# Optimization experiments

Measured on AMD Instinct MI355X. Metric: run time of the kernel, lower is better.

Reference implementation:

```python
import jax, jax.numpy as jnp
import numpy as np

B, S, D, E = 4, 2048, 512, 32

def setup_inputs() -> dict:
    key = jax.random.key(0)
    k1, k2, k3 = jax.random.split(key, 3)
    x = jax.random.normal(k1, (B, S, D), dtype=jnp.float32)
    # glorot-ish scaling for weights
    gate_w = jax.random.normal(k2, (D, E), dtype=jnp.float32) * (1.0 / np.sqrt(D))
    gate_b = jnp.zeros((E,), dtype=jnp.float32)
    expert_w = jax.random.normal(k3, (E, D, D), dtype=jnp.float32) * (1.0 / np.sqrt(D))
    return {"x": x, "gate_w": gate_w, "gate_b": gate_b, "expert_w": expert_w}

def reference(x, gate_w, gate_b, expert_w):
    # gate_scores: [B,S,E] (context=None -> route on x itself)
    gate = jax.nn.softmax(jnp.einsum('bsd,de->bse', x, gate_w) + gate_b, axis=-1)
    # Dense soft-MoE: sum_e gate[b,s,e] * (x[b,s,:] @ expert_w[e])
    # Single einsum avoids materializing the [B,S,E,D] intermediate.
    out = jnp.einsum('bse,bsd,edf->bsf', gate, x, expert_w)
    return out
```

## Files before the change

### kernel.cpp

```cpp
#include <hip/hip_runtime.h>

#define TOK 8192
#define DIM 512
#define NE  32
#define KTOT (NE * DIM)

#define BM 128
#define BN 64
#define BK 64

typedef float f32x4 __attribute__((ext_vector_type(4)));
typedef short s16x8 __attribute__((ext_vector_type(8)));

typedef const void __attribute__((address_space(1)))* gp1_t;
typedef void __attribute__((address_space(3)))* lp3_t;

__device__ __forceinline__ void gl_lds16(const void* g, void* l) {
    __builtin_amdgcn_global_load_lds((gp1_t)g, (lp3_t)l, 16, 0, 0);
}

__device__ __forceinline__ ushort f2bf(float f) {
    unsigned u = __builtin_bit_cast(unsigned, f);
    unsigned r = (u + 0x7fffu + ((u >> 16) & 1u)) >> 16;
    return (ushort)r;
}

__global__ __launch_bounds__(256) void k_prep(const float* __restrict__ w,
                                              ushort* __restrict__ wt,
                                              const float* __restrict__ x,
                                              const float* __restrict__ gw,
                                              const float* __restrict__ gb,
                                              float* __restrict__ G2,
                                              ushort* __restrict__ xb) {
    __shared__ __align__(16) char smem[64 * 65 * 4];
    const int bx = blockIdx.x;
    const int tid = threadIdx.x;
    if (bx < 2048) {
        float (*tile)[65] = (float(*)[65])smem;
        const int e = bx >> 6;
        const int f0 = ((bx >> 3) & 7) * 64;
        const int d0 = (bx & 7) * 64;
        const int tx = tid & 63, ty = tid >> 6;
        const float* we = w + (size_t)e * DIM * DIM;
#pragma unroll
        for (int i = ty; i < 64; i += 4)
            tile[i][tx] = we[(size_t)(d0 + i) * DIM + f0 + tx];
        __syncthreads();
#pragma unroll
        for (int i = ty; i < 64; i += 4)
            wt[(size_t)(f0 + i) * KTOT + e * DIM + d0 + tx] = f2bf(tile[tx][i]);
    } else {
        float* xs = (float*)smem;
        const int t0 = (bx - 2048) * 8;
        const float* xBase = x + (size_t)t0 * DIM;
#pragma unroll
        for (int k = 0; k < 4; ++k) {
            int i4 = (k * 256 + tid) * 4;
            float4 v = *(const float4*)(xBase + i4);
            xs[i4 + 0] = v.x; xs[i4 + 1] = v.y; xs[i4 + 2] = v.z; xs[i4 + 3] = v.w;
            ushort4 o;
            o.x = f2bf(v.x); o.y = f2bf(v.y); o.z = f2bf(v.z); o.w = f2bf(v.w);
            *(ushort4*)(xb + (size_t)t0 * DIM + i4) = o;
        }
        __syncthreads();
        const int tok = tid >> 5;
        const int e = tid & 31;
        float l = gb[e];
        const float* xr = xs + tok * DIM;
#pragma unroll 8
        for (int d = 0; d < DIM; ++d)
            l += xr[d] * gw[d * NE + e];
        float mx = l;
#pragma unroll
        for (int m = 16; m >= 1; m >>= 1) mx = fmaxf(mx, __shfl_xor(mx, m));
        float ex = expf(l - mx);
        float s = ex;
#pragma unroll
        for (int m = 16; m >= 1; m >>= 1) s += __shfl_xor(s, m);
        G2[(size_t)e * TOK + t0 + tok] = ex / s;
    }
}

__global__ __launch_bounds__(256, 4) void k_moe_gemm(const ushort* __restrict__ xb,
                                                     const ushort* __restrict__ wt,
                                                     const float* __restrict__ G2,
                                                     float* __restrict__ out0,
                                                     float* __restrict__ out1) {
    __shared__ __align__(16) ushort Bs[2][BN * BK];
    __shared__ float Gs[16][BM];

    const int tid = threadIdx.x;
    const int m0 = blockIdx.y * BM;
    const int n0 = blockIdx.x * BN;
    const int e0 = blockIdx.z * 16;
    float* __restrict__ dst = blockIdx.z ? out1 : out0;

    for (int i = tid; i < 16 * BM; i += 256) {
        int e = i >> 7, r = i & 127;
        Gs[e][r] = G2[(size_t)(e0 + e) * TOK + m0 + r];
    }

    const int lane = tid & 63;
    const int wave = tid >> 6;
    const int wm = (wave & 1) * 64;
    const int wn = (wave >> 1) * 32;
    const int l15 = lane & 15;
    const int q = lane >> 4;
    const int keyR = l15 & 7;

    int rb[2][2];
#pragma unroll
    for (int j = 0; j < 2; ++j)
#pragma unroll
        for (int ks = 0; ks < 2; ++ks)
            rb[j][ks] = (wn + j * 16 + l15) * 128 + (((ks * 4 + q) ^ keyR) << 4);

    const int srow = tid >> 3;
    const int c8 = tid & 7;
    const int scol = ((c8 ^ (srow & 7)) * 8);
    const ushort* bBase = wt + (size_t)(n0 + srow) * KTOT + (size_t)e0 * DIM + scol;
    const ushort* bBase2 = bBase + (size_t)32 * KTOT;
    const int ldsOff = tid * 16;

    const ushort* aP[4];
#pragma unroll
    for (int i = 0; i < 4; ++i)
        aP[i] = xb + (size_t)(m0 + wm + i * 16 + l15) * DIM + q * 8;

    const f32x4 zv = {0.f, 0.f, 0.f, 0.f};
    f32x4 acc[4][2];
#pragma unroll
    for (int i = 0; i < 4; ++i)
#pragma unroll
        for (int j = 0; j < 2; ++j) acc[i][j] = zv;

    gl_lds16(bBase, (char*)Bs[0] + ldsOff);
    gl_lds16(bBase2, (char*)Bs[0] + 4096 + ldsOff);
    __syncthreads();

#pragma unroll 1
    for (int kt = 0; kt < 8; ++kt) {
        s16x8 a[4][2];
#pragma unroll
        for (int i = 0; i < 4; ++i) {
            a[i][0] = *(const s16x8*)(aP[i] + kt * 64);
            a[i][1] = *(const s16x8*)(aP[i] + kt * 64 + 32);
        }

#pragma unroll 1
        for (int ee = 0; ee < 16; ++ee) {
            const int g = kt * 16 + ee;
            if (g + 1 < 128) {
                const int gn = g + 1;
                const ushort* bN = bBase + (size_t)(gn & 15) * DIM + (gn >> 4) * BK;
                char* bL = (char*)Bs[gn & 1] + ldsOff;
                gl_lds16(bN, bL);
                gl_lds16(bN + (size_t)32 * KTOT, bL + 4096);
            }

            const char* Bb = (const char*)Bs[g & 1];
            s16x8 b[2][2];
#pragma unroll
            for (int j = 0; j < 2; ++j) {
                b[j][0] = *(const s16x8*)(Bb + rb[j][0]);
                b[j][1] = *(const s16x8*)(Bb + rb[j][1]);
            }

#pragma unroll
            for (int i = 0; i < 4; ++i) {
                const f32x4 gt = *(const f32x4*)&Gs[ee][wm + i * 16 + q * 4];
#pragma unroll
                for (int j = 0; j < 2; ++j) {
                    f32x4 p = __builtin_amdgcn_mfma_f32_16x16x32_bf16(
                        a[i][0], b[j][0], zv, 0, 0, 0);
                    p = __builtin_amdgcn_mfma_f32_16x16x32_bf16(
                        a[i][1], b[j][1], p, 0, 0, 0);
                    acc[i][j][0] += gt[0] * p[0];
                    acc[i][j][1] += gt[1] * p[1];
                    acc[i][j][2] += gt[2] * p[2];
                    acc[i][j][3] += gt[3] * p[3];
                }
            }
            __syncthreads();
        }
    }

#pragma unroll
    for (int i = 0; i < 4; ++i) {
        const int tl = m0 + wm + i * 16 + q * 4;
#pragma unroll
        for (int j = 0; j < 2; ++j) {
            const int f = n0 + wn + j * 16 + l15;
            float* p = dst + (size_t)tl * DIM + f;
            p[0 * DIM] = acc[i][j][0];
            p[1 * DIM] = acc[i][j][1];
            p[2 * DIM] = acc[i][j][2];
            p[3 * DIM] = acc[i][j][3];
        }
    }
}

__global__ __launch_bounds__(256) void k_reduce(float* __restrict__ out,
                                                const float* __restrict__ P) {
    int i = (blockIdx.x * 256 + threadIdx.x) * 4;
    float4 a = *(const float4*)(out + i);
    float4 b = *(const float4*)(P + i);
    a.x += b.x; a.y += b.y; a.z += b.z; a.w += b.w;
    *(float4*)(out + i) = a;
}

extern "C" void kernel_launch(void* const* d_in, const int* in_sizes, int n_in,
                              void* d_out, int out_size, void* d_ws, size_t ws_size,
                              hipStream_t stream) {
    const float* x  = (const float*)d_in[0];
    const float* gw = (const float*)d_in[1];
    const float* gb = (const float*)d_in[2];
    const float* w  = (const float*)d_in[3];
    float* out = (float*)d_out;

    char* ws = (char*)d_ws;
    ushort* xb = (ushort*)ws;
    ushort* wt = (ushort*)(ws + (8u << 20));
    float*  G2 = (float*)(ws + (24u << 20));
    float*  P  = (float*)(ws + (25u << 20));

    k_prep<<<dim3(2048 + TOK / 8), dim3(256), 0, stream>>>(w, wt, x, gw, gb, G2, xb);
    k_moe_gemm<<<dim3(DIM / BN, TOK / BM, 2), dim3(256), 0, stream>>>(xb, wt, G2, out, P);
    k_reduce<<<dim3(TOK * DIM / 1024), dim3(256), 0, stream>>>(out, P);
}
```

Before: 273.2 us.

## Reorder MoE GEMM loop to accumulate full expert K before gate scaling

Reorders the GEMM loops so each expert's full 512-wide K reduction runs as a chain of MFMAs into a partial accumulator, with the gate scaling applied once per expert rather than after every 64-wide K slice. This cuts the per-slice VALU multiply-adds and lets MFMAs chain without zero-initialised accumulators. B tiles now load two K slices per stage, halving the barriers, and gate values are stored as bf16 to shrink shared memory. The costs are more accumulator registers, bigger LDS use that could lower occupancy, A fragments reloaded from global on every expert, and the precision lost by rounding gates to bf16.

```diff
diff --git a/kernel.cpp b/kernel.cpp
--- a/kernel.cpp
+++ b/kernel.cpp
@@ -23,6 +23,10 @@
     unsigned u = __builtin_bit_cast(unsigned, f);
     unsigned r = (u + 0x7fffu + ((u >> 16) & 1u)) >> 16;
     return (ushort)r;
+}
+
+__device__ __forceinline__ float bf2f(ushort u) {
+    return __builtin_bit_cast(float, (unsigned)u << 16);
 }
 
 __global__ __launch_bounds__(256) void k_prep(const float* __restrict__ w,
@@ -30,7 +34,7 @@
                                               const float* __restrict__ x,
                                               const float* __restrict__ gw,
                                               const float* __restrict__ gb,
-                                              float* __restrict__ G2,
+                                              ushort* __restrict__ G2b,
                                               ushort* __restrict__ xb) {
     __shared__ __align__(16) char smem[64 * 65 * 4];
     const int bx = blockIdx.x;
@@ -77,17 +81,17 @@
         float s = ex;
 #pragma unroll
         for (int m = 16; m >= 1; m >>= 1) s += __shfl_xor(s, m);
-        G2[(size_t)e * TOK + t0 + tok] = ex / s;
+        G2b[(size_t)e * TOK + t0 + tok] = f2bf(ex / s);
     }
 }
 
 __global__ __launch_bounds__(256, 4) void k_moe_gemm(const ushort* __restrict__ xb,
                                                      const ushort* __restrict__ wt,
-                                                     const float* __restrict__ G2,
+                                                     const ushort* __restrict__ G2b,
                                                      float* __restrict__ out0,
                                                      float* __restrict__ out1) {
-    __shared__ __align__(16) ushort Bs[2][BN * BK];
-    __shared__ float Gs[16][BM];
+    __shared__ __align__(16) ushort Bs[2][2][BN * BK];
+    __shared__ ushort Gs[16][BM];
 
     const int tid = threadIdx.x;
     const int m0 = blockIdx.y * BM;
@@ -95,10 +99,8 @@
     const int e0 = blockIdx.z * 16;
     float* __restrict__ dst = blockIdx.z ? out1 : out0;
 
-    for (int i = tid; i < 16 * BM; i += 256) {
-        int e = i >> 7, r = i & 127;
-        Gs[e][r] = G2[(size_t)(e0 + e) * TOK + m0 + r];
-    }
+    for (int i = tid; i < 16 * BM; i += 256)
+        Gs[i >> 7][i & 127] = G2b[(size_t)(e0 + (i >> 7)) * TOK + m0 + (i & 127)];
 
     const int lane = tid & 63;
     const int wave = tid >> 6;
@@ -119,7 +121,6 @@
     const int c8 = tid & 7;
     const int scol = ((c8 ^ (srow & 7)) * 8);
     const ushort* bBase = wt + (size_t)(n0 + srow) * KTOT + (size_t)e0 * DIM + scol;
-    const ushort* bBase2 = bBase + (size_t)32 * KTOT;
     const int ldsOff = tid * 16;
 
     const ushort* aP[4];
@@ -134,54 +135,97 @@
 #pragma unroll
         for (int j = 0; j < 2; ++j) acc[i][j] = zv;
 
-    gl_lds16(bBase, (char*)Bs[0] + ldsOff);
-    gl_lds16(bBase2, (char*)Bs[0] + 4096 + ldsOff);
+#pragma unroll
+    for (int t = 0; t < 2; ++t) {
+        const ushort* src = bBase + t * BK;
+        gl_lds16(src, (char*)Bs[0][t] + ldsOff);
+        gl_lds16(src + (size_t)32 * KTOT, (char*)Bs[0][t] + 4096 + ldsOff);
+    }
     __syncthreads();
 
 #pragma unroll 1
-    for (int kt = 0; kt < 8; ++kt) {
-        s16x8 a[4][2];
+    for (int ee = 0; ee < 16; ++ee) {
+        f32x4 pacc[4][2];
+#pragma unroll
+        for (int i = 0; i < 4; ++i)
+#pragma unroll
+            for (int j = 0; j < 2; ++j) pacc[i][j] = zv;
+
+#pragma unroll 1
+        for (int kp = 0; kp < 4; ++kp) {
+            const int p = ee * 4 + kp;
+            const int kt0 = kp * 2;
+
+            s16x8 a[4][2];
+#pragma unroll
+            for (int i = 0; i < 4; ++i) {
+                a[i][0] = *(const s16x8*)(aP[i] + kt0 * 64);
+                a[i][1] = *(const s16x8*)(aP[i] + kt0 * 64 + 32);
+            }
+
+            if (p + 1 < 64) {
+                const int en = (p + 1) >> 2;
+                const int kpn = (p + 1) & 3;
+                char* bl = (char*)Bs[(p + 1) & 1];
+#pragma unroll
+                for (int t = 0; t < 2; ++t) {
+                    const ushort* src = bBase + (size_t)en * DIM + (kpn * 2 + t) * BK;
+                    gl_lds16(src, bl + t * 8192 + ldsOff);
+                    gl_lds16(src + (size_t)32 * KTOT, bl + t * 8192 + 4096 + ldsOff);
+                }
+            }
+
+            {
+                const char* Bb = (const char*)Bs[p & 1][0];
+#pragma unroll
+                for (int ks = 0; ks < 2; ++ks) {
+                    s16x8 b0 = *(const s16x8*)(Bb + rb[0][ks]);
+                    s16x8 b1 = *(const s16x8*)(Bb + rb[1][ks]);
+#pragma unroll
+                    for (int i = 0; i < 4; ++i) {
+                        pacc[i][0] = __builtin_amdgcn_mfma_f32_16x16x32_bf16(
+                            a[i][ks], b0, pacc[i][0], 0, 0, 0);
+                        pacc[i][1] = __builtin_amdgcn_mfma_f32_16x16x32_bf16(
+                            a[i][ks], b1, pacc[i][1], 0, 0, 0);
+                    }
+                }
+            }
+
+#pragma unroll
+            for (int i = 0; i < 4; ++i) {
+                a[i][0] = *(const s16x8*)(aP[i] + kt0 * 64 + 64);
+                a[i][1] = *(const s16x8*)(aP[i] + kt0 * 64 + 96);
+            }
+            {
+                const char* Bb = (const char*)Bs[p & 1][1];
+#pragma unroll
+                for (int ks = 0; ks < 2; ++ks) {
+                    s16x8 b0 = *(const s16x8*)(Bb + rb[0][ks]);
+                    s16x8 b1 = *(const s16x8*)(Bb + rb[1][ks]);
+#pragma unroll
+                    for (int i = 0; i < 4; ++i) {
+                        pacc[i][0] = __builtin_amdgcn_mfma_f32_16x16x32_bf16(
+                            a[i][ks], b0, pacc[i][0], 0, 0, 0);
+                        pacc[i][1] = __builtin_amdgcn_mfma_f32_16x16x32_bf16(
+                            a[i][ks], b1, pacc[i][1], 0, 0, 0);
+                    }
+                }
+            }
+            __syncthreads();
+        }
+
 #pragma unroll
         for (int i = 0; i < 4; ++i) {
-            a[i][0] = *(const s16x8*)(aP[i] + kt * 64);
-            a[i][1] = *(const s16x8*)(aP[i] + kt * 64 + 32);
-        }
-
-#pragma unroll 1
-        for (int ee = 0; ee < 16; ++ee) {
-            const int g = kt * 16 + ee;
-            if (g + 1 < 128) {
-                const int gn = g + 1;
-                const ushort* bN = bBase + (size_t)(gn & 15) * DIM + (gn >> 4) * BK;
-                char* bL = (char*)Bs[gn & 1] + ldsOff;
-                gl_lds16(bN, bL);
-                gl_lds16(bN + (size_t)32 * KTOT, bL + 4096);
-            }
-
-            const char* Bb = (const char*)Bs[g & 1];
-            s16x8 b[2][2];
+            const ushort4 gu = *(const ushort4*)&Gs[ee][wm + i * 16 + q * 4];
+            const float g0 = bf2f(gu.x), g1 = bf2f(gu.y);
+            const float g2 = bf2f(gu.z), g3 = bf2f(gu.w);
 #pragma unroll
             for (int j = 0; j < 2; ++j) {
-                b[j][0] = *(const s16x8*)(Bb + rb[j][0]);
-                b[j][1] = *(const s16x8*)(Bb + rb[j][1]);
-            }
-
-#pragma unroll
-            for (int i = 0; i < 4; ++i) {
-                const f32x4 gt = *(const f32x4*)&Gs[ee][wm + i * 16 + q * 4];
-#pragma unroll
-                for (int j = 0; j < 2; ++j) {
-                    f32x4 p = __builtin_amdgcn_mfma_f32_16x16x32_bf16(
-                        a[i][0], b[j][0], zv, 0, 0, 0);
-                    p = __builtin_amdgcn_mfma_f32_16x16x32_bf16(
-                        a[i][1], b[j][1], p, 0, 0, 0);
-                    acc[i][j][0] += gt[0] * p[0];
-                    acc[i][j][1] += gt[1] * p[1];
-                    acc[i][j][2] += gt[2] * p[2];
-                    acc[i][j][3] += gt[3] * p[3];
-                }
-            }
-            __syncthreads();
+                acc[i][j][0] += g0 * pacc[i][j][0];
+                acc[i][j][1] += g1 * pacc[i][j][1];
+                acc[i][j][2] += g2 * pacc[i][j][2];
+                acc[i][j][3] += g3 * pacc[i][j][3];
+            }
         }
     }
 
@@ -219,12 +263,12 @@
     float* out = (float*)d_out;
 
     char* ws = (char*)d_ws;
-    ushort* xb = (ushort*)ws;
-    ushort* wt = (ushort*)(ws + (8u << 20));
-    float*  G2 = (float*)(ws + (24u << 20));
-    float*  P  = (float*)(ws + (25u << 20));
-
-    k_prep<<<dim3(2048 + TOK / 8), dim3(256), 0, stream>>>(w, wt, x, gw, gb, G2, xb);
-    k_moe_gemm<<<dim3(DIM / BN, TOK / BM, 2), dim3(256), 0, stream>>>(xb, wt, G2, out, P);
+    ushort* xb  = (ushort*)ws;
+    ushort* wt  = (ushort*)(ws + (8u << 20));
+    ushort* G2b = (ushort*)(ws + (24u << 20));
+    float*  P   = (float*)(ws + (25u << 20));
+
+    k_prep<<<dim3(2048 + TOK / 8), dim3(256), 0, stream>>>(w, wt, x, gw, gb, G2b, xb);
+    k_moe_gemm<<<dim3(DIM / BN, TOK / BM, 2), dim3(256), 0, stream>>>(xb, wt, G2b, out, P);
     k_reduce<<<dim3(TOK * DIM / 1024), dim3(256), 0, stream>>>(out, P);
 }
```

Result: slower. 609.1 us (+123.0%).
